# Optimization experiments

Measured on AMD Instinct MI355X. Metric: run time of the kernel, lower is better.

## Reference

```python
import jax, jax.numpy as jnp
import numpy as np

ACT_BITS = 8
W_BITS = 8
BN_EPS = 1e-5


def _round_ste(x):
    # straight-through round (HAWQ-style ste_round)
    return x + jax.lax.stop_gradient(jnp.round(x) - x)


def _quant_sym(x, bits):
    # symmetric per-tensor fake quantization; scale treated as constant (EMA min/max in original)
    n = float(2 ** (bits - 1) - 1)
    s = jax.lax.stop_gradient(jnp.maximum(jnp.max(jnp.abs(x)) / n, 1e-8))
    xq = jnp.clip(_round_ste(x / s), -n - 1.0, n) * s
    return xq, s


def _conv(x, w, stride, pad):
    return jax.lax.conv_general_dilated(
        x, w, (stride, stride), [(pad, pad), (pad, pad)],
        dimension_numbers=("NCHW", "OIHW", "NCHW"))


def _quant_bn(x, gamma, beta, mean, var):
    # fold BN into a per-channel scale+bias; quantize the folded scale like a weight
    ws = gamma * jax.lax.rsqrt(var + BN_EPS)          # [C]
    wq, ws_scale = _quant_sym(ws, W_BITS)
    b = beta - mean * wq                               # [C]
    return x * wq[None, :, None, None] + b[None, :, None, None], ws_scale


def setup_inputs() -> dict:
    key = jax.random.key(0)
    ks = jax.random.split(key, 16)
    d = {}
    d["x"] = jax.random.normal(ks[0], (32, 128, 56, 56), jnp.float32)
    d["w1"] = jax.random.normal(ks[1], (256, 128, 3, 3), jnp.float32) * 0.05
    d["w2"] = jax.random.normal(ks[2], (256, 256, 3, 3), jnp.float32) * 0.05
    d["w_id"] = jax.random.normal(ks[3], (256, 128, 1, 1), jnp.float32) * 0.05
    for i, pfx in enumerate(["bn1", "bn2", "id"]):
        k4 = jax.random.split(ks[4 + i], 4)
        d[pfx + "_gamma"] = jax.random.uniform(k4[0], (256,), jnp.float32) + 0.5
        d[pfx + "_beta"] = jax.random.normal(k4[1], (256,), jnp.float32) * 0.1
        d[pfx + "_mean"] = jax.random.normal(k4[2], (256,), jnp.float32) * 0.1
        d[pfx + "_var"] = jax.random.uniform(k4[3], (256,), jnp.float32) + 0.5
    return d


def reference(x, w1, w2, w_id,
              bn1_gamma, bn1_beta, bn1_mean, bn1_var,
              bn2_gamma, bn2_beta, bn2_mean, bn2_var,
              id_gamma, id_beta, id_mean, id_var):
    # quant_act on block input
    xq, act_s = _quant_sym(x, ACT_BITS)

    # identity branch: 1x1 stride-2 quantized conv -> quant_act -> folded quant bn
    w_id_q, _ = _quant_sym(w_id, W_BITS)
    identity = _conv(xq, w_id_q, 2, 0)
    identity, _ = _quant_sym(identity, ACT_BITS)
    identity, _ = _quant_bn(identity, id_gamma, id_beta, id_mean, id_var)

    # main branch conv1 (3x3 stride 2) -> act quant -> bn -> relu -> act quant
    w1_q, _ = _quant_sym(w1, W_BITS)
    h = _conv(xq, w1_q, 2, 1)
    h, _ = _quant_sym(h, ACT_BITS)
    h, _ = _quant_bn(h, bn1_gamma, bn1_beta, bn1_mean, bn1_var)
    h = jax.nn.relu(h)
    h, _ = _quant_sym(h, ACT_BITS)

    # conv2 (3x3 stride 1) -> act quant -> bn
    w2_q, _ = _quant_sym(w2, W_BITS)
    h = _conv(h, w2_q, 1, 1)
    h, _ = _quant_sym(h, ACT_BITS)
    h, _ = _quant_bn(h, bn2_gamma, bn2_beta, bn2_mean, bn2_var)

    # residual add -> int32 requant -> relu
    h = h + identity
    h, out_s = _quant_sym(h, ACT_BITS)
    h = jax.nn.relu(h)
    return h, out_s
```

## Files before the change

### kernel.cpp

```cpp
#include <hip/hip_runtime.h>
#include <limits.h>

#define THREADS 256
#define GRID_BLOCKS 896

typedef int vi4 __attribute__((ext_vector_type(4)));

__device__ __forceinline__ float clamp8f(float q) { return fminf(fmaxf(q, -128.0f), 127.0f); }
__device__ __forceinline__ float sc_from_bits(unsigned b) {
  return fmaxf(__uint_as_float(b) / 127.0f, 1e-8f);
}
__device__ __forceinline__ signed char q8(float v, float s) {
  return (signed char)(int)clamp8f(rintf(v / s));
}


__device__ __forceinline__ void gbar(int* IS, int base, int bx) {
  asm volatile("s_waitcnt vmcnt(0)" ::: "memory");
  int old = __hip_atomic_fetch_add(IS + base + (bx & 7) * 16, 1, __ATOMIC_RELAXED,
                                   __HIP_MEMORY_SCOPE_AGENT);
  if (old == 111) {
    int r = __hip_atomic_fetch_add(IS + base + 128, 1, __ATOMIC_RELAXED, __HIP_MEMORY_SCOPE_AGENT);
    if (r == 7)
      __hip_atomic_fetch_add(IS + base + 144, 1, __ATOMIC_RELAXED, __HIP_MEMORY_SCOPE_AGENT);
  }
  while (__hip_atomic_load(IS + base + 144, __ATOMIC_RELAXED, __HIP_MEMORY_SCOPE_SYSTEM) == 0)
    __builtin_amdgcn_s_sleep(2);
}

__device__ __forceinline__ void amax_body(const float4* __restrict__ p, int n4, int bid,
                                          int nblocks, int* __restrict__ slot) {
  const int tid = threadIdx.x;
  const int stride = nblocks * THREADS;
  float m = 0.0f;
  int i = bid * THREADS + tid;
  for (; i + 3 * stride < n4; i += 4 * stride) {
    float4 v0 = p[i];
    float4 v1 = p[i + stride];
    float4 v2 = p[i + 2 * stride];
    float4 v3 = p[i + 3 * stride];
    float m0 = fmaxf(fmaxf(fabsf(v0.x), fabsf(v0.y)), fmaxf(fabsf(v0.z), fabsf(v0.w)));
    float m1 = fmaxf(fmaxf(fabsf(v1.x), fabsf(v1.y)), fmaxf(fabsf(v1.z), fabsf(v1.w)));
    float m2 = fmaxf(fmaxf(fabsf(v2.x), fabsf(v2.y)), fmaxf(fabsf(v2.z), fabsf(v2.w)));
    float m3 = fmaxf(fmaxf(fabsf(v3.x), fabsf(v3.y)), fmaxf(fabsf(v3.z), fabsf(v3.w)));
    m = fmaxf(m, fmaxf(fmaxf(m0, m1), fmaxf(m2, m3)));
  }
  for (; i < n4; i += stride) {
    float4 v = p[i];
    m = fmaxf(m, fmaxf(fmaxf(fabsf(v.x), fabsf(v.y)), fmaxf(fabsf(v.z), fabsf(v.w))));
  }
#pragma unroll
  for (int k = 32; k >= 1; k >>= 1) m = fmaxf(m, __shfl_xor(m, k));
  __shared__ float wred[4];
  if ((tid & 63) == 0) wred[tid >> 6] = m;
  __syncthreads();
  if (tid == 0) {
    m = fmaxf(fmaxf(wred[0], wred[1]), fmaxf(wred[2], wred[3]));
    atomicMax(slot, __float_as_int(m));
  }
}

__global__ __launch_bounds__(THREADS) void k_pre(
    int* IS, const float* g1, const float* be1, const float* m1, const float* v1, float* wq1,
    float* b1, const float* g2, const float* be2, const float* m2, const float* v2, float* wq2,
    float* b2, const float* gi, const float* bei, const float* mi, const float* vvi, float* wqi,
    float* bi, const float4* w1, const float4* w2, const float4* wid, const float4* x) {
  int b = blockIdx.x;
  int c = threadIdx.x;
  if (b < 3) {
    if (b == 0) {
      IS[128 + c] = 0;
      IS[384 + c] = 0;
      IS[640 + c] = 0;
      if (c < 32) IS[896 + c] = 0;
    }
    const float *gamma, *beta, *mean, *var;
    float *wq, *bb;
    if (b == 0) { gamma = g1; beta = be1; mean = m1; var = v1; wq = wq1; bb = b1; }
    else if (b == 1) { gamma = g2; beta = be2; mean = m2; var = v2; wq = wq2; bb = b2; }
    else { gamma = gi; beta = bei; mean = mi; var = vvi; wq = wqi; bb = bi; }
    __shared__ float red[THREADS];
    float ws = gamma[c] * (1.0f / sqrtf(var[c] + 1e-5f));
    red[c] = fabsf(ws);
    __syncthreads();
    for (int s = THREADS / 2; s > 0; s >>= 1) {
      if (c < s) red[c] = fmaxf(red[c], red[c + s]);
      __syncthreads();
    }
    float sws = fmaxf(red[0] / 127.0f, 1e-8f);
    float q = clamp8f(rintf(ws / sws)) * sws;
    wq[c] = q;
    bb[c] = beta[c] - mean[c] * q;
    return;
  }
  b -= 3;
  if (b < 64) { amax_body(w1, 73728, b, 64, IS + 1); return; }
  b -= 64;
  if (b < 128) { amax_body(w2, 147456, b, 128, IS + 2); return; }
  b -= 128;
  if (b < 16) { amax_body(wid, 8192, b, 16, IS + 3); return; }
  b -= 16;
  amax_body(x, 3211264, b, 512, IS + 0);
}

__global__ __launch_bounds__(THREADS) void k_quant(const float* __restrict__ x,
                                                   int* __restrict__ X8,
                                                   const float* __restrict__ w1f,
                                                   vi4* __restrict__ W1m,
                                                   const float* __restrict__ w2f,
                                                   vi4* __restrict__ W2m,
                                                   const float* __restrict__ widf,
                                                   vi4* __restrict__ Widm,
                                                   const unsigned* __restrict__ ISu) {
  __shared__ signed char tile[56 * 132];
  int b = blockIdx.x;
  int t = threadIdx.x;
  if (b < 1792) {
    float s = sc_from_bits(ISu[0]);
    int h = b % 56, n = b / 56;
    const float* xp = x + ((n * 128) * 56 + h) * 56;
#pragma unroll
    for (int k = 0; k < 28; ++k) {
      int i = t + k * 256;
      int w = i % 56, c = i / 56;
      tile[w * 132 + c] = q8(xp[c * 3136 + w], s);
    }
    __syncthreads();
    int* op = X8 + (n * 56 + h) * 56 * 32;
#pragma unroll
    for (int k = 0; k < 7; ++k) {
      int i = t + k * 256;
      int w = i >> 5, c4 = (i & 31) * 4;
      const signed char* tp = tile + w * 132 + c4;
      op[i] = (int)(unsigned char)tp[0] | ((int)(unsigned char)tp[1] << 8) |
              ((int)(unsigned char)tp[2] << 16) | ((int)(unsigned char)tp[3] << 24);
    }
    return;
  }
  if (b < 1864) {
    int tt = (b - 1792) * THREADS + t;
    float s = sc_from_bits(ISu[1]);
    int lane = tt & 63;
    int cotile = (tt >> 6) & 15;
    int ks = tt >> 10;
    int tap = ks >> 1, kc = ks & 1;
    int kh = tap / 3, kw = tap % 3;
    int co = cotile * 16 + (lane & 15);
    int ci0 = kc * 64 + (lane >> 4) * 16;
    const float* src = w1f + (co * 128 + ci0) * 9 + kh * 3 + kw;
    int r[4];
#pragma unroll
    for (int q = 0; q < 4; ++q) {
      unsigned b0 = (unsigned char)q8(src[(q * 4 + 0) * 9], s);
      unsigned b1 = (unsigned char)q8(src[(q * 4 + 1) * 9], s);
      unsigned b2 = (unsigned char)q8(src[(q * 4 + 2) * 9], s);
      unsigned b3 = (unsigned char)q8(src[(q * 4 + 3) * 9], s);
      r[q] = (int)(b0 | (b1 << 8) | (b2 << 16) | (b3 << 24));
    }
    vi4 v = {r[0], r[1], r[2], r[3]};
    W1m[tt] = v;
    return;
  }
  if (b < 2008) {
    int tt = (b - 1864) * THREADS + t;
    float s = sc_from_bits(ISu[2]);
    int lane = tt & 63;
    int cotile = (tt >> 6) & 15;
    int ks = tt >> 10;
    int tap = ks >> 2, kc = ks & 3;
    int kh = tap / 3, kw = tap % 3;
    int co = cotile * 16 + (lane & 15);
    int ci0 = kc * 64 + (lane >> 4) * 16;
    const float* src = w2f + (co * 256 + ci0) * 9 + kh * 3 + kw;
    int r[4];
#pragma unroll
    for (int q = 0; q < 4; ++q) {
      unsigned b0 = (unsigned char)q8(src[(q * 4 + 0) * 9], s);
      unsigned b1 = (unsigned char)q8(src[(q * 4 + 1) * 9], s);
      unsigned b2 = (unsigned char)q8(src[(q * 4 + 2) * 9], s);
      unsigned b3 = (unsigned char)q8(src[(q * 4 + 3) * 9], s);
      r[q] = (int)(b0 | (b1 << 8) | (b2 << 16) | (b3 << 24));
    }
    vi4 v = {r[0], r[1], r[2], r[3]};
    W2m[tt] = v;
    return;
  }
  {
    int tt = (b - 2008) * THREADS + t;
    float s = sc_from_bits(ISu[3]);
    int lane = tt & 63;
    int cotile = (tt >> 6) & 15;
    int ks = tt >> 10;
    int co = cotile * 16 + (lane & 15);
    int ci0 = ks * 64 + (lane >> 4) * 16;
    const float* src = widf + co * 128 + ci0;
    int r[4];
#pragma unroll
    for (int q = 0; q < 4; ++q) {
      unsigned b0 = (unsigned char)q8(src[q * 4 + 0], s);
      unsigned b1 = (unsigned char)q8(src[q * 4 + 1], s);
      unsigned b2 = (unsigned char)q8(src[q * 4 + 2], s);
      unsigned b3 = (unsigned char)q8(src[q * 4 + 3], s);
      r[q] = (int)(b0 | (b1 << 8) | (b2 << 16) | (b3 << 24));
    }
    vi4 v = {r[0], r[1], r[2], r[3]};
    Widm[tt] = v;
  }
}

#define MFMA_I8(a, b, c) __builtin_amdgcn_mfma_i32_16x16x64_i8(a, b, c, 0, 0, 0)

__device__ __forceinline__ signed char qact(int v, float sxw, float s_h1, float s_y2, float wq,
                                            float bb) {
  float hf = (float)v * sxw;
  float q = clamp8f(rintf(hf / s_h1));
  float hv = q * s_h1;
  float y = fmaxf(hv * wq + bb, 0.0f);
  float a = fminf(fmaxf(rintf(y / s_y2), -128.0f), 127.0f);
  return (signed char)(int)a;
}

__device__ __forceinline__ float sc_slot(const int* IS, int slot) {
  unsigned u = (unsigned)__hip_atomic_load((int*)(IS + slot), __ATOMIC_RELAXED,
                                           __HIP_MEMORY_SCOPE_AGENT);
  return fmaxf(__uint_as_float(u) / 127.0f, 1e-8f);
}

__global__ __launch_bounds__(THREADS, 4) void k_cv1(const int* X8, const vi4* __restrict__ W1m,
                                                    const vi4* __restrict__ Widm,
                                                    int* __restrict__ IDI, int* A2i, int* IS,
                                                    const float* __restrict__ wq1,
                                                    const float* __restrict__ b1, float* SC,
                                                    int* maxS2, int* minS2) {
  __shared__ __align__(16) int lds[9280];
  __shared__ int redA[4];
  __shared__ int sVmax, sVmin;
  __shared__ float sSxw, sSh1, sSy2;
  const int tid = threadIdx.x;
  const int bx = blockIdx.x;
  const int n = bx / 28, rr = bx % 28;
  const int hp = rr >> 1, nh = rr & 1;
  const int ho0 = hp * 2;
  vi4 zero = {0, 0, 0, 0};

  for (int r = 0; r < 5; ++r) {
    int h = 2 * ho0 - 1 + r;
    int* dst = lds + r * 58 * 32;
    if (h >= 0 && h < 56) {
      const vi4* src = (const vi4*)(X8 + (n * 56 + h) * 56 * 32);
      for (int i4 = tid; i4 < 448; i4 += THREADS) {
        int col = i4 >> 3, e0 = (i4 & 7) * 4;
        int cell = r * 58 + col + 1;
        *(vi4*)(lds + cell * 32 + (e0 ^ ((cell & 7) << 2))) = src[i4];
      }
      if (tid < 32) dst[tid] = 0;
      else if (tid >= 128 && tid < 160) dst[57 * 32 + (tid - 128)] = 0;
    } else {
      for (int i4 = tid; i4 < 464; i4 += THREADS) ((vi4*)dst)[i4] = zero;
    }
  }
  __syncthreads();

  const int lane = tid & 63, wv = tid >> 6;
  const int mw = wv & 1, nw = wv >> 1;
  const int lm = lane & 15, quad = lane >> 4;
  const int woc0 = lm, woc1 = (16 + lm) > 27 ? 27 : (16 + lm);
  const int choff = quad * 4;
  const int ho = ho0 + mw;
  const int obase = ((n * 28 + ho) * 28) * 256;
  const int ctbase = nh * 8 + nw * 4;

#define LDA(row, colp, sub)                                                              \
  (*(const vi4*)(lds + ((row) * 58 + (colp)) * 32 +                                      \
                 ((sub) ^ ((((row) * 58 + (colp)) & 7) << 2))))

  vi4 acc[2][4];
  vi4 bA[4], bB[4];
  vi4 a0A, a1A, a0B, a1B;

#pragma unroll
  for (int mt = 0; mt < 2; ++mt)
#pragma unroll
    for (int ct = 0; ct < 4; ++ct) acc[mt][ct] = zero;
  const vi4* wibase = Widm + ctbase * 64 + lane;
  {
    const int row = 2 * mw + 1;
#pragma unroll
    for (int kc = 0; kc < 2; ++kc) {
      vi4 a0 = LDA(row, 2 * woc0 + 1, kc * 16 + choff);
      vi4 a1 = LDA(row, 2 * woc1 + 1, kc * 16 + choff);
#pragma unroll
      for (int ct = 0; ct < 4; ++ct) {
        vi4 b = wibase[kc * 1024 + ct * 64];
        acc[0][ct] = MFMA_I8(a0, b, acc[0][ct]);
        acc[1][ct] = MFMA_I8(a1, b, acc[1][ct]);
      }
    }
  }
  int am = 0;
#pragma unroll
  for (int ct = 0; ct < 4; ++ct) {
    const int co = (ctbase + ct) * 16 + lm;
#pragma unroll
    for (int mt = 0; mt < 2; ++mt)
#pragma unroll
      for (int r = 0; r < 4; ++r) {
        int wo = mt * 16 + quad * 4 + r;
        if (wo < 28) {
          int v = acc[mt][ct][r];
          IDI[obase + wo * 256 + co] = v;
          am = max(am, v < 0 ? -v : v);
        }
      }
  }
#pragma unroll
  for (int k = 32; k >= 1; k >>= 1) am = max(am, __shfl_xor(am, k));
  if (lane == 0) redA[wv] = am;

#pragma unroll
  for (int mt = 0; mt < 2; ++mt)
#pragma unroll
    for (int ct = 0; ct < 4; ++ct) acc[mt][ct] = zero;
  const vi4* wbase = W1m + ctbase * 64 + lane;
#pragma unroll
  for (int ct = 0; ct < 4; ++ct) bA[ct] = wbase[ct * 64];
  {
    a0A = LDA(2 * mw, 2 * woc0, choff);
    a1A = LDA(2 * mw, 2 * woc1, choff);
  }
#pragma unroll 1
  for (int ks = 0; ks < 18; ks += 2) {
    {
      const int ksn = ks + 1;
      const int khn = (ksn >= 6) + (ksn >= 12);
      const int t2 = ksn - khn * 6;
      const int kwn = t2 >> 1, kcn = t2 & 1;
#pragma unroll
      for (int ct = 0; ct < 4; ++ct) bB[ct] = wbase[ksn * 1024 + ct * 64];
      const int row = 2 * mw + khn;
      a0B = LDA(row, 2 * woc0 + kwn, kcn * 16 + choff);
      a1B = LDA(row, 2 * woc1 + kwn, kcn * 16 + choff);
    }
#pragma unroll
    for (int ct = 0; ct < 4; ++ct) {
      acc[0][ct] = MFMA_I8(a0A, bA[ct], acc[0][ct]);
      acc[1][ct] = MFMA_I8(a1A, bA[ct], acc[1][ct]);
    }
    if (ks + 2 < 18) {
      const int ksn = ks + 2;
      const int khn = (ksn >= 6) + (ksn >= 12);
      const int t2 = ksn - khn * 6;
      const int kwn = t2 >> 1, kcn = t2 & 1;
#pragma unroll
      for (int ct = 0; ct < 4; ++ct) bA[ct] = wbase[ksn * 1024 + ct * 64];
      const int row = 2 * mw + khn;
      a0A = LDA(row, 2 * woc0 + kwn, kcn * 16 + choff);
      a1A = LDA(row, 2 * woc1 + kwn, kcn * 16 + choff);
    }
#pragma unroll
    for (int ct = 0; ct < 4; ++ct) {
      acc[0][ct] = MFMA_I8(a0B, bB[ct], acc[0][ct]);
      acc[1][ct] = MFMA_I8(a1B, bB[ct], acc[1][ct]);
    }
  }

#pragma unroll
  for (int ct = 0; ct < 4; ++ct) {
    int vmax = INT_MIN, vmin = INT_MAX;
#pragma unroll
    for (int mt = 0; mt < 2; ++mt)
#pragma unroll
      for (int r = 0; r < 4; ++r) {
        int wo = mt * 16 + quad * 4 + r;
        if (wo < 28) {
          int v = acc[mt][ct][r];
          vmax = max(vmax, v);
          vmin = min(vmin, v);
        }
      }
    vmax = max(vmax, __shfl_xor(vmax, 16));
    vmax = max(vmax, __shfl_xor(vmax, 32));
    vmin = min(vmin, __shfl_xor(vmin, 16));
    vmin = min(vmin, __shfl_xor(vmin, 32));
    if (lane < 16) {
      int cl = (nw * 4 + ct) * 16 + lane;
      __hip_atomic_store(maxS2 + bx * 256 + mw * 128 + cl, vmax, __ATOMIC_RELAXED,
                         __HIP_MEMORY_SCOPE_AGENT);
      __hip_atomic_store(minS2 + bx * 256 + mw * 128 + cl, vmin, __ATOMIC_RELAXED,
                         __HIP_MEMORY_SCOPE_AGENT);
    }
  }

  __syncthreads();
  if (tid == 0) {
    int a = max(max(redA[0], redA[1]), max(redA[2], redA[3]));
    atomicMax(IS + 5, a);
  }
#pragma unroll
  for (int ct = 0; ct < 4; ++ct) {
    const int cl = (nw * 4 + ct) * 16 + lm;
#pragma unroll
    for (int mt = 0; mt < 2; ++mt)
#pragma unroll
      for (int r = 0; r < 4; ++r) {
        int wo = mt * 16 + quad * 4 + r;
        if (wo < 28) lds[(mw * 28 + wo) * 130 + cl] = acc[mt][ct][r];
      }
  }
  __syncthreads();
  if (tid == 0) gbar(IS, 128, bx);
  __syncthreads();

  if (bx < 256) {
    const int c = bx, nhc = c >> 7, cl = c & 127;
    int vmax = INT_MIN, vmin = INT_MAX;
    for (int j = tid; j < 896; j += THREADS) {
      int bxx = nhc + ((j >> 1) << 1);
      int mwj = j & 1;
      int a = __hip_atomic_load(maxS2 + bxx * 256 + mwj * 128 + cl, __ATOMIC_RELAXED,
                                __HIP_MEMORY_SCOPE_AGENT);
      int i_ = __hip_atomic_load(minS2 + bxx * 256 + mwj * 128 + cl, __ATOMIC_RELAXED,
                                 __HIP_MEMORY_SCOPE_AGENT);
      vmax = max(vmax, a);
      vmin = min(vmin, i_);
    }
    int* rMax = lds + 7280;
    int* rMin = lds + 7536;
    rMax[tid] = vmax;
    rMin[tid] = vmin;
    __syncthreads();
    for (int s = 128; s > 0; s >>= 1) {
      if (tid < s) {
        rMax[tid] = max(rMax[tid], rMax[tid + s]);
        rMin[tid] = min(rMin[tid], rMin[tid + s]);
      }
      __syncthreads();
    }
    if (tid == 0) {
      sVmax = rMax[0];
      sVmin = rMin[0];
      int a1 = sVmax < 0 ? -sVmax : sVmax;
      int a0 = sVmin < 0 ? -sVmin : sVmin;
      atomicMax(IS + 4, max(a1, a0));
    }
  }
  __syncthreads();
  if (tid == 0) gbar(IS, 288, bx);
  __syncthreads();

  if (bx < 256 && tid == 0) {
    float sx = sc_slot(IS, 0);
    float sw1 = sc_slot(IS, 1);
    int mh1 = __hip_atomic_load(IS + 4, __ATOMIC_RELAXED, __HIP_MEMORY_SCOPE_AGENT);
    float sxw = sx * sw1;
    float s_h1 = fmaxf(sxw * (float)mh1 / 127.0f, 1e-8f);
    float wq = wq1[bx], bbc = b1[bx];
    float q1 = clamp8f(rintf((float)sVmax * sxw / s_h1));
    float q0 = clamp8f(rintf((float)sVmin * sxw / s_h1));
    float y1 = fmaxf(q1 * s_h1 * wq + bbc, 0.0f);
    float y0 = fmaxf(q0 * s_h1 * wq + bbc, 0.0f);
    atomicMax(IS + 7, __float_as_int(fmaxf(y1, y0)));
  }
  __syncthreads();
  if (tid == 0) gbar(IS, 448, bx);
  __syncthreads();

  if (tid == 0) {
    float sx = sc_slot(IS, 0);
    float sw1 = sc_slot(IS, 1);
    int mh1 = __hip_atomic_load(IS + 4, __ATOMIC_RELAXED, __HIP_MEMORY_SCOPE_AGENT);
    int mrf = __hip_atomic_load(IS + 7, __ATOMIC_RELAXED, __HIP_MEMORY_SCOPE_AGENT);
    float sxw = sx * sw1;
    float s_h1 = fmaxf(sxw * (float)mh1 / 127.0f, 1e-8f);
    float s_y2 = fmaxf(__int_as_float(mrf) / 127.0f, 1e-8f);
    sSxw = sxw;
    sSh1 = s_h1;
    sSy2 = s_y2;
    if (bx == 0) {
      int mid = __hip_atomic_load(IS + 5, __ATOMIC_RELAXED, __HIP_MEMORY_SCOPE_AGENT);
      float swid = sc_slot(IS, 3);
      SC[9] = s_y2;
      SC[10] = fmaxf(sx * swid * (float)mid / 127.0f, 1e-8f);
    }
  }
  __syncthreads();

  {
    const float sxw = sSxw, s_h1 = sSh1, s_y2 = sSy2;
#pragma unroll
    for (int k = 0; k < 7; ++k) {
      int i = tid + k * 256;
      int sp = i >> 5, c4i = i & 31;
      int mwp = sp >= 28 ? 1 : 0;
      int wo = sp - mwp * 28;
      int c0 = nh * 128 + c4i * 4;
      const int* pk = lds + sp * 130 + c4i * 4;
      unsigned r0 = (unsigned char)qact(pk[0], sxw, s_h1, s_y2, wq1[c0], b1[c0]);
      unsigned r1 = (unsigned char)qact(pk[1], sxw, s_h1, s_y2, wq1[c0 + 1], b1[c0 + 1]);
      unsigned r2 = (unsigned char)qact(pk[2], sxw, s_h1, s_y2, wq1[c0 + 2], b1[c0 + 2]);
      unsigned r3 = (unsigned char)qact(pk[3], sxw, s_h1, s_y2, wq1[c0 + 3], b1[c0 + 3]);
      A2i[((n * 28 + ho0 + mwp) * 28 + wo) * 64 + nh * 32 + c4i] =
          (int)(r0 | (r1 << 8) | (r2 << 16) | (r3 << 24));
    }
  }
#undef LDA
}

struct SumParams {
  float sxw2, s_h2, sxwid, s_idq;
};
__device__ __forceinline__ float sum_val(int v2, int vi, const SumParams& P, float wq2c, float b2c,
                                         float wqidc, float bidc) {
  float q2 = clamp8f(rintf((float)v2 * P.sxw2 / P.s_h2));
  float z = (q2 * P.s_h2) * wq2c + b2c;
  float qi = clamp8f(rintf((float)vi * P.sxwid / P.s_idq));
  float zi = (qi * P.s_idq) * wqidc + bidc;
  return z + zi;
}
__device__ __forceinline__ SumParams make_params2(const float* SC, const unsigned* ISu, int mh2) {
  SumParams P;
  float sx = sc_from_bits(ISu[0]);
  float sw2 = sc_from_bits(ISu[2]);
  float swid = sc_from_bits(ISu[3]);
  float s_y2 = SC[9];
  P.s_idq = SC[10];
  P.sxw2 = s_y2 * sw2;
  P.s_h2 = fmaxf(P.sxw2 * (float)mh2 / 127.0f, 1e-8f);
  P.sxwid = sx * swid;
  return P;
}

__global__ __launch_bounds__(THREADS, 4) void k_tail(const int* __restrict__ A2,
                                                     const vi4* __restrict__ W2m,
                                                     const int* __restrict__ IDI,
                                                     const float* SC, int* IS,
                                                     const float* __restrict__ wq2,
                                                     const float* __restrict__ b2,
                                                     const float* __restrict__ wqid,
                                                     const float* __restrict__ bidp,
                                                     float* __restrict__ out) {
  __shared__ __align__(16) int lds[4 * 30 * 68];
  __shared__ int redA[4];
  __shared__ float redF[4];
  __shared__ int sMh2;
  __shared__ float sOutS;
  const int tid = threadIdx.x;
  const int bx = blockIdx.x;
  const int n = bx / 28, rr = bx % 28;
  const int hp = rr >> 1, nh = rr & 1;
  const int ho0 = hp * 2;
  vi4 zero = {0, 0, 0, 0};

  for (int r = 0; r < 4; ++r) {
    int h = ho0 - 1 + r;
    int* dst = lds + r * 30 * 68;
    if (h >= 0 && h < 28) {
      const vi4* src = (const vi4*)(A2 + (n * 28 + h) * 28 * 64);
      for (int i4 = tid; i4 < 448; i4 += THREADS) {
        int col = i4 >> 4, c = (i4 & 15) * 4;
        *(vi4*)(dst + (col + 1) * 68 + c) = src[i4];
      }
      if (tid < 64) dst[tid] = 0;
      else if (tid >= 128 && tid < 192) dst[29 * 68 + (tid - 128)] = 0;
    } else {
      for (int i4 = tid; i4 < 510; i4 += THREADS) ((vi4*)dst)[i4] = zero;
    }
  }
  __syncthreads();

  const int lane = tid & 63, wv = tid >> 6;
  const int mw = wv & 1, nw = wv >> 1;
  const int lm = lane & 15, quad = lane >> 4;
  const int woc0 = lm, woc1 = (16 + lm) > 27 ? 27 : (16 + lm);
  const int choff = quad * 4;
  const int ctbase = nh * 8 + nw * 4;

  vi4 acc[2][4];
  vi4 bA[4], bB[4];
  vi4 a0A, a1A, a0B, a1B;
#pragma unroll
  for (int mt = 0; mt < 2; ++mt)
#pragma unroll
    for (int ct = 0; ct < 4; ++ct) acc[mt][ct] = zero;

  const vi4* wbase = W2m + ctbase * 64 + lane;
#pragma unroll
  for (int ct = 0; ct < 4; ++ct) bA[ct] = wbase[ct * 64];
  {
    const int ro = mw * 30;
    a0A = *(const vi4*)(lds + (ro + woc0) * 68 + choff);
    a1A = *(const vi4*)(lds + (ro + woc1) * 68 + choff);
  }
#pragma unroll 1
  for (int ks = 0; ks < 36; ks += 2) {
    {
      const int ksn = ks + 1;
      const int khn = (ksn >= 12) + (ksn >= 24);
      const int t2 = ksn - khn * 12;
      const int kwn = t2 >> 2, kcn = t2 & 3;
#pragma unroll
      for (int ct = 0; ct < 4; ++ct) bB[ct] = wbase[ksn * 1024 + ct * 64];
      const int ro = (mw + khn) * 30;
      a0B = *(const vi4*)(lds + (ro + woc0 + kwn) * 68 + kcn * 16 + choff);
      a1B = *(const vi4*)(lds + (ro + woc1 + kwn) * 68 + kcn * 16 + choff);
    }
#pragma unroll
    for (int ct = 0; ct < 4; ++ct) {
      acc[0][ct] = MFMA_I8(a0A, bA[ct], acc[0][ct]);
      acc[1][ct] = MFMA_I8(a1A, bA[ct], acc[1][ct]);
    }
    if (ks + 2 < 36) {
      const int ksn = ks + 2;
      const int khn = (ksn >= 12) + (ksn >= 24);
      const int t2 = ksn - khn * 12;
      const int kwn = t2 >> 2, kcn = t2 & 3;
#pragma unroll
      for (int ct = 0; ct < 4; ++ct) bA[ct] = wbase[ksn * 1024 + ct * 64];
      const int ro = (mw + khn) * 30;
      a0A = *(const vi4*)(lds + (ro + woc0 + kwn) * 68 + kcn * 16 + choff);
      a1A = *(const vi4*)(lds + (ro + woc1 + kwn) * 68 + kcn * 16 + choff);
    }
#pragma unroll
    for (int ct = 0; ct < 4; ++ct) {
      acc[0][ct] = MFMA_I8(a0B, bB[ct], acc[0][ct]);
      acc[1][ct] = MFMA_I8(a1B, bB[ct], acc[1][ct]);
    }
  }

  int am = 0;
#pragma unroll
  for (int ct = 0; ct < 4; ++ct)
#pragma unroll
    for (int mt = 0; mt < 2; ++mt)
#pragma unroll
      for (int r = 0; r < 4; ++r) {
        int wo = mt * 16 + quad * 4 + r;
        if (wo < 28) {
          int v = acc[mt][ct][r];
          am = max(am, v < 0 ? -v : v);
        }
      }
#pragma unroll
  for (int k = 32; k >= 1; k >>= 1) am = max(am, __shfl_xor(am, k));
  if (lane == 0) redA[wv] = am;
  __syncthreads();
  if (tid == 0) {
    int a = max(max(redA[0], redA[1]), max(redA[2], redA[3]));
    atomicMax(IS + 6, a);
  }

  int* sumsi = lds;
  float* sums = (float*)lds;
  const int ib = ((n * 28 + ho0) * 28) * 256 + nh * 128;
#pragma unroll
  for (int k = 0; k < 28; ++k) {
    int idx = tid + k * 256;
    int cl = idx & 127, sp = idx >> 7;
    sumsi[cl * 57 + sp] = IDI[ib + sp * 256 + cl];
  }
  __syncthreads();
  if (tid == 0) {
    gbar(IS, 608, bx);
    sMh2 = __hip_atomic_load(IS + 6, __ATOMIC_RELAXED, __HIP_MEMORY_SCOPE_SYSTEM);
  }
  __syncthreads();
  const SumParams P = make_params2(SC, (const unsigned*)IS, sMh2);

  float fm = 0.0f;
#pragma unroll
  for (int ct = 0; ct < 4; ++ct) {
    const int co = (ctbase + ct) * 16 + lm;
    const int cl = co - nh * 128;
    float w2c = wq2[co], b2c = b2[co], wic = wqid[co], bic = bidp[co];
#pragma unroll
    for (int mt = 0; mt < 2; ++mt)
#pragma unroll
      for (int r = 0; r < 4; ++r) {
        int wo = mt * 16 + quad * 4 + r;
        if (wo < 28) {
          int slot = cl * 57 + mw * 28 + wo;
          float sv = sum_val(acc[mt][ct][r], sumsi[slot], P, w2c, b2c, wic, bic);
          sums[slot] = sv;
          fm = fmaxf(fm, fabsf(sv));
        }
      }
  }
#pragma unroll
  for (int k = 32; k >= 1; k >>= 1) fm = fmaxf(fm, __shfl_xor(fm, k));
  if (lane == 0) redF[wv] = fm;
  __syncthreads();
  if (tid == 0) {
    float a = fmaxf(fmaxf(redF[0], redF[1]), fmaxf(redF[2], redF[3]));
    atomicMax(IS + 11, __float_as_int(a));
    gbar(IS, 768, bx);
    int mb = __hip_atomic_load(IS + 11, __ATOMIC_RELAXED, __HIP_MEMORY_SCOPE_SYSTEM);
    sOutS = fmaxf(__int_as_float(mb) / 127.0f, 1e-8f);
  }
  __syncthreads();
  const float out_s = sOutS;

  float* ob = out + n * 200704 + (nh * 128) * 784 + ho0 * 28;
#pragma unroll
  for (int k = 0; k < 28; ++k) {
    int idx = tid + k * 256;
    int cl = idx / 56, rem = idx % 56;
    float sv = sums[cl * 57 + rem];
    float q = clamp8f(rintf(sv / out_s));
    ob[cl * 784 + rem] = q > 0.0f ? q * out_s : 0.0f;
  }
  if (bx == 0 && tid == 0) out[6422528] = out_s;
}

extern "C" void kernel_launch(void* const* d_in, const int* in_sizes, int n_in, void* d_out,
                              int out_size, void* d_ws, size_t ws_size, hipStream_t stream) {
  (void)in_sizes; (void)n_in; (void)out_size; (void)ws_size;
  const float* x = (const float*)d_in[0];
  const float* w1 = (const float*)d_in[1];
  const float* w2 = (const float*)d_in[2];
  const float* wid = (const float*)d_in[3];
  const float* bn1g = (const float*)d_in[4];
  const float* bn1b = (const float*)d_in[5];
  const float* bn1m = (const float*)d_in[6];
  const float* bn1v = (const float*)d_in[7];
  const float* bn2g = (const float*)d_in[8];
  const float* bn2b = (const float*)d_in[9];
  const float* bn2m = (const float*)d_in[10];
  const float* bn2v = (const float*)d_in[11];
  const float* idg = (const float*)d_in[12];
  const float* idb = (const float*)d_in[13];
  const float* idm = (const float*)d_in[14];
  const float* idv = (const float*)d_in[15];

  char* ws = (char*)d_ws;
  float* SC = (float*)ws;
  int* IS = (int*)ws;
  unsigned* ISu = (unsigned*)ws;
  float* wq1 = (float*)(ws + 4096);
  float* b1 = (float*)(ws + 5120);
  float* wq2 = (float*)(ws + 6144);
  float* b2 = (float*)(ws + 7168);
  float* wqid = (float*)(ws + 8192);
  float* bid = (float*)(ws + 9216);
  char* X8 = ws + 16384;
  char* A2 = X8;
  char* W1m = X8 + 12845056;
  char* W2m = W1m + 294912;
  char* Widm = W2m + 589824;
  int* IDI = (int*)(Widm + 32768);
  float* out = (float*)d_out;
  int* maxS2 = (int*)d_out;
  int* minS2 = maxS2 + 896 * 256;

  k_pre<<<723, THREADS, 0, stream>>>(IS, bn1g, bn1b, bn1m, bn1v, wq1, b1, bn2g, bn2b, bn2m, bn2v,
                                     wq2, b2, idg, idb, idm, idv, wqid, bid, (const float4*)w1,
                                     (const float4*)w2, (const float4*)wid, (const float4*)x);
  k_quant<<<2016, THREADS, 0, stream>>>(x, (int*)X8, w1, (vi4*)W1m, w2, (vi4*)W2m, wid,
                                        (vi4*)Widm, ISu);
  k_cv1<<<GRID_BLOCKS, THREADS, 0, stream>>>((const int*)X8, (const vi4*)W1m, (const vi4*)Widm,
                                             IDI, (int*)A2, IS, wq1, b1, SC, maxS2, minS2);
  k_tail<<<GRID_BLOCKS, THREADS, 0, stream>>>((const int*)A2, (const vi4*)W2m, (const int*)IDI, SC,
                                              IS, wq2, b2, wqid, bid, out);
}
```

Measured before the change: 249.8 us.

## Fuse conv1 and tail kernels into one persistent kernel, keep identity in registers

Merges the conv1 kernel and the conv2/residual tail kernel into a single persistent kernel. A grid barrier separates the A2 activation write from the conv2 halo read. The identity-branch int32 accumulators now stay in registers across the whole kernel instead of round-tripping through the IDI global buffer, and the scale parameters stay in shared memory instead of the SC slots. This removes one kernel launch and the IDI write and read traffic, in exchange for higher register pressure from the extra accumulators and an added grid-wide barrier that relies on all 896 blocks being co-resident.

```diff
diff --git a/kernel.cpp b/kernel.cpp
--- a/kernel.cpp
+++ b/kernel.cpp
@@ -72,7 +72,7 @@
       IS[128 + c] = 0;
       IS[384 + c] = 0;
       IS[640 + c] = 0;
-      if (c < 32) IS[896 + c] = 0;
+      if (c < 192) IS[896 + c] = 0;
     }
     const float *gamma, *beta, *mean, *var;
     float *wq, *bb;
@@ -226,16 +226,31 @@
   return fmaxf(__uint_as_float(u) / 127.0f, 1e-8f);
 }
 
-__global__ __launch_bounds__(THREADS, 4) void k_cv1(const int* X8, const vi4* __restrict__ W1m,
-                                                    const vi4* __restrict__ Widm,
-                                                    int* __restrict__ IDI, int* A2i, int* IS,
-                                                    const float* __restrict__ wq1,
-                                                    const float* __restrict__ b1, float* SC,
-                                                    int* maxS2, int* minS2) {
+struct SumParams {
+  float sxw2, s_h2, sxwid, s_idq;
+};
+__device__ __forceinline__ float sum_val(int v2, int vi, const SumParams& P, float wq2c, float b2c,
+                                         float wqidc, float bidc) {
+  float q2 = clamp8f(rintf((float)v2 * P.sxw2 / P.s_h2));
+  float z = (q2 * P.s_h2) * wq2c + b2c;
+  float qi = clamp8f(rintf((float)vi * P.sxwid / P.s_idq));
+  float zi = (qi * P.s_idq) * wqidc + bidc;
+  return z + zi;
+}
+
+__global__ __launch_bounds__(THREADS, 4) void k_ct(
+    const int* X8, const vi4* __restrict__ W1m, const vi4* __restrict__ Widm,
+    const vi4* __restrict__ W2m, int* A2p, int* IS, const float* __restrict__ wq1,
+    const float* __restrict__ b1, const float* __restrict__ wq2, const float* __restrict__ b2,
+    const float* __restrict__ wqid, const float* __restrict__ bidp, float* __restrict__ out,
+    int* maxS2, int* minS2) {
   __shared__ __align__(16) int lds[9280];
-  __shared__ int redA[4];
+  __shared__ int redA[4], redH[4];
   __shared__ int sVmax, sVmin;
-  __shared__ float sSxw, sSh1, sSy2;
+  __shared__ float redF[4];
+  __shared__ float sSxw, sSh1, sSy2, sSxwid, sSidq, sSxw2;
+  __shared__ int sMh2;
+  __shared__ float sOutS;
   const int tid = threadIdx.x;
   const int bx = blockIdx.x;
   const int n = bx / 28, rr = bx % 28;
@@ -266,8 +281,6 @@
   const int lm = lane & 15, quad = lane >> 4;
   const int woc0 = lm, woc1 = (16 + lm) > 27 ? 27 : (16 + lm);
   const int choff = quad * 4;
-  const int ho = ho0 + mw;
-  const int obase = ((n * 28 + ho) * 28) * 256;
   const int ctbase = nh * 8 + nw * 4;
 
 #define LDA(row, colp, sub)                                                              \
@@ -275,13 +288,14 @@
                  ((sub) ^ ((((row) * 58 + (colp)) & 7) << 2))))
 
   vi4 acc[2][4];
+  vi4 accI[2][4];
   vi4 bA[4], bB[4];
   vi4 a0A, a1A, a0B, a1B;
 
 #pragma unroll
   for (int mt = 0; mt < 2; ++mt)
 #pragma unroll
-    for (int ct = 0; ct < 4; ++ct) acc[mt][ct] = zero;
+    for (int ct = 0; ct < 4; ++ct) accI[mt][ct] = zero;
   const vi4* wibase = Widm + ctbase * 64 + lane;
   {
     const int row = 2 * mw + 1;
@@ -292,27 +306,24 @@
 #pragma unroll
       for (int ct = 0; ct < 4; ++ct) {
         vi4 b = wibase[kc * 1024 + ct * 64];
-        acc[0][ct] = MFMA_I8(a0, b, acc[0][ct]);
-        acc[1][ct] = MFMA_I8(a1, b, acc[1][ct]);
+        accI[0][ct] = MFMA_I8(a0, b, accI[0][ct]);
+        accI[1][ct] = MFMA_I8(a1, b, accI[1][ct]);
       }
     }
   }
   int am = 0;
 #pragma unroll
-  for (int ct = 0; ct < 4; ++ct) {
-    const int co = (ctbase + ct) * 16 + lm;
+  for (int ct = 0; ct < 4; ++ct)
 #pragma unroll
     for (int mt = 0; mt < 2; ++mt)
 #pragma unroll
       for (int r = 0; r < 4; ++r) {
         int wo = mt * 16 + quad * 4 + r;
         if (wo < 28) {
-          int v = acc[mt][ct][r];
-          IDI[obase + wo * 256 + co] = v;
+          int v = accI[mt][ct][r];
           am = max(am, v < 0 ? -v : v);
         }
       }
-  }
 #pragma unroll
   for (int k = 32; k >= 1; k >>= 1) am = max(am, __shfl_xor(am, k));
   if (lane == 0) redA[wv] = am;
@@ -363,6 +374,7 @@
       acc[1][ct] = MFMA_I8(a1B, bB[ct], acc[1][ct]);
     }
   }
+#undef LDA
 
 #pragma unroll
   for (int ct = 0; ct < 4; ++ct) {
@@ -471,17 +483,15 @@
     int mh1 = __hip_atomic_load(IS + 4, __ATOMIC_RELAXED, __HIP_MEMORY_SCOPE_AGENT);
     int mrf = __hip_atomic_load(IS + 7, __ATOMIC_RELAXED, __HIP_MEMORY_SCOPE_AGENT);
     float sxw = sx * sw1;
-    float s_h1 = fmaxf(sxw * (float)mh1 / 127.0f, 1e-8f);
+    sSxw = sxw;
+    sSh1 = fmaxf(sxw * (float)mh1 / 127.0f, 1e-8f);
     float s_y2 = fmaxf(__int_as_float(mrf) / 127.0f, 1e-8f);
-    sSxw = sxw;
-    sSh1 = s_h1;
     sSy2 = s_y2;
-    if (bx == 0) {
-      int mid = __hip_atomic_load(IS + 5, __ATOMIC_RELAXED, __HIP_MEMORY_SCOPE_AGENT);
-      float swid = sc_slot(IS, 3);
-      SC[9] = s_y2;
-      SC[10] = fmaxf(sx * swid * (float)mid / 127.0f, 1e-8f);
-    }
+    int mid = __hip_atomic_load(IS + 5, __ATOMIC_RELAXED, __HIP_MEMORY_SCOPE_AGENT);
+    float swid = sc_slot(IS, 3);
+    sSxwid = sx * swid;
+    sSidq = fmaxf(sx * swid * (float)mid / 127.0f, 1e-8f);
+    sSxw2 = s_y2 * sc_slot(IS, 2);
   }
   __syncthreads();
 
@@ -499,63 +509,20 @@
       unsigned r1 = (unsigned char)qact(pk[1], sxw, s_h1, s_y2, wq1[c0 + 1], b1[c0 + 1]);
       unsigned r2 = (unsigned char)qact(pk[2], sxw, s_h1, s_y2, wq1[c0 + 2], b1[c0 + 2]);
       unsigned r3 = (unsigned char)qact(pk[3], sxw, s_h1, s_y2, wq1[c0 + 3], b1[c0 + 3]);
-      A2i[((n * 28 + ho0 + mwp) * 28 + wo) * 64 + nh * 32 + c4i] =
-          (int)(r0 | (r1 << 8) | (r2 << 16) | (r3 << 24));
-    }
-  }
-#undef LDA
-}
-
-struct SumParams {
-  float sxw2, s_h2, sxwid, s_idq;
-};
-__device__ __forceinline__ float sum_val(int v2, int vi, const SumParams& P, float wq2c, float b2c,
-                                         float wqidc, float bidc) {
-  float q2 = clamp8f(rintf((float)v2 * P.sxw2 / P.s_h2));
-  float z = (q2 * P.s_h2) * wq2c + b2c;
-  float qi = clamp8f(rintf((float)vi * P.sxwid / P.s_idq));
-  float zi = (qi * P.s_idq) * wqidc + bidc;
-  return z + zi;
-}
-__device__ __forceinline__ SumParams make_params2(const float* SC, const unsigned* ISu, int mh2) {
-  SumParams P;
-  float sx = sc_from_bits(ISu[0]);
-  float sw2 = sc_from_bits(ISu[2]);
-  float swid = sc_from_bits(ISu[3]);
-  float s_y2 = SC[9];
-  P.s_idq = SC[10];
-  P.sxw2 = s_y2 * sw2;
-  P.s_h2 = fmaxf(P.sxw2 * (float)mh2 / 127.0f, 1e-8f);
-  P.sxwid = sx * swid;
-  return P;
-}
-
-__global__ __launch_bounds__(THREADS, 4) void k_tail(const int* __restrict__ A2,
-                                                     const vi4* __restrict__ W2m,
-                                                     const int* __restrict__ IDI,
-                                                     const float* SC, int* IS,
-                                                     const float* __restrict__ wq2,
-                                                     const float* __restrict__ b2,
-                                                     const float* __restrict__ wqid,
-                                                     const float* __restrict__ bidp,
-                                                     float* __restrict__ out) {
-  __shared__ __align__(16) int lds[4 * 30 * 68];
-  __shared__ int redA[4];
-  __shared__ float redF[4];
-  __shared__ int sMh2;
-  __shared__ float sOutS;
-  const int tid = threadIdx.x;
-  const int bx = blockIdx.x;
-  const int n = bx / 28, rr = bx % 28;
-  const int hp = rr >> 1, nh = rr & 1;
-  const int ho0 = hp * 2;
-  vi4 zero = {0, 0, 0, 0};
+      __hip_atomic_store(A2p + ((n * 28 + ho0 + mwp) * 28 + wo) * 64 + nh * 32 + c4i,
+                         (int)(r0 | (r1 << 8) | (r2 << 16) | (r3 << 24)), __ATOMIC_RELAXED,
+                         __HIP_MEMORY_SCOPE_AGENT);
+    }
+  }
+  __syncthreads();
+  if (tid == 0) gbar(IS, 608, bx);
+  __syncthreads();
 
   for (int r = 0; r < 4; ++r) {
     int h = ho0 - 1 + r;
     int* dst = lds + r * 30 * 68;
     if (h >= 0 && h < 28) {
-      const vi4* src = (const vi4*)(A2 + (n * 28 + h) * 28 * 64);
+      const vi4* src = (const vi4*)(A2p + (n * 28 + h) * 28 * 64);
       for (int i4 = tid; i4 < 448; i4 += THREADS) {
         int col = i4 >> 4, c = (i4 & 15) * 4;
         *(vi4*)(dst + (col + 1) * 68 + c) = src[i4];
@@ -568,24 +535,13 @@
   }
   __syncthreads();
 
-  const int lane = tid & 63, wv = tid >> 6;
-  const int mw = wv & 1, nw = wv >> 1;
-  const int lm = lane & 15, quad = lane >> 4;
-  const int woc0 = lm, woc1 = (16 + lm) > 27 ? 27 : (16 + lm);
-  const int choff = quad * 4;
-  const int ctbase = nh * 8 + nw * 4;
-
-  vi4 acc[2][4];
-  vi4 bA[4], bB[4];
-  vi4 a0A, a1A, a0B, a1B;
 #pragma unroll
   for (int mt = 0; mt < 2; ++mt)
 #pragma unroll
     for (int ct = 0; ct < 4; ++ct) acc[mt][ct] = zero;
-
-  const vi4* wbase = W2m + ctbase * 64 + lane;
-#pragma unroll
-  for (int ct = 0; ct < 4; ++ct) bA[ct] = wbase[ct * 64];
+  const vi4* wbase2 = W2m + ctbase * 64 + lane;
+#pragma unroll
+  for (int ct = 0; ct < 4; ++ct) bA[ct] = wbase2[ct * 64];
   {
     const int ro = mw * 30;
     a0A = *(const vi4*)(lds + (ro + woc0) * 68 + choff);
@@ -599,7 +555,7 @@
       const int t2 = ksn - khn * 12;
       const int kwn = t2 >> 2, kcn = t2 & 3;
 #pragma unroll
-      for (int ct = 0; ct < 4; ++ct) bB[ct] = wbase[ksn * 1024 + ct * 64];
+      for (int ct = 0; ct < 4; ++ct) bB[ct] = wbase2[ksn * 1024 + ct * 64];
       const int ro = (mw + khn) * 30;
       a0B = *(const vi4*)(lds + (ro + woc0 + kwn) * 68 + kcn * 16 + choff);
       a1B = *(const vi4*)(lds + (ro + woc1 + kwn) * 68 + kcn * 16 + choff);
@@ -615,7 +571,7 @@
       const int t2 = ksn - khn * 12;
       const int kwn = t2 >> 2, kcn = t2 & 3;
 #pragma unroll
-      for (int ct = 0; ct < 4; ++ct) bA[ct] = wbase[ksn * 1024 + ct * 64];
+      for (int ct = 0; ct < 4; ++ct) bA[ct] = wbase2[ksn * 1024 + ct * 64];
       const int ro = (mw + khn) * 30;
       a0A = *(const vi4*)(lds + (ro + woc0 + kwn) * 68 + kcn * 16 + choff);
       a1A = *(const vi4*)(lds + (ro + woc1 + kwn) * 68 + kcn * 16 + choff);
@@ -627,7 +583,7 @@
     }
   }
 
-  int am = 0;
+  int am2 = 0;
 #pragma unroll
   for (int ct = 0; ct < 4; ++ct)
 #pragma unroll
@@ -637,35 +593,27 @@
         int wo = mt * 16 + quad * 4 + r;
         if (wo < 28) {
           int v = acc[mt][ct][r];
-          am = max(am, v < 0 ? -v : v);
+          am2 = max(am2, v < 0 ? -v : v);
         }
       }
 #pragma unroll
-  for (int k = 32; k >= 1; k >>= 1) am = max(am, __shfl_xor(am, k));
-  if (lane == 0) redA[wv] = am;
+  for (int k = 32; k >= 1; k >>= 1) am2 = max(am2, __shfl_xor(am2, k));
+  if (lane == 0) redH[wv] = am2;
   __syncthreads();
   if (tid == 0) {
-    int a = max(max(redA[0], redA[1]), max(redA[2], redA[3]));
-    atomicMax(IS + 6, a);
-  }
-
-  int* sumsi = lds;
+    atomicMax(IS + 6, max(max(redH[0], redH[1]), max(redH[2], redH[3])));
+    gbar(IS, 768, bx);
+    sMh2 = __hip_atomic_load(IS + 6, __ATOMIC_RELAXED, __HIP_MEMORY_SCOPE_SYSTEM);
+  }
+  __syncthreads();
+
+  SumParams P;
+  P.sxw2 = sSxw2;
+  P.s_h2 = fmaxf(sSxw2 * (float)sMh2 / 127.0f, 1e-8f);
+  P.sxwid = sSxwid;
+  P.s_idq = sSidq;
+
   float* sums = (float*)lds;
-  const int ib = ((n * 28 + ho0) * 28) * 256 + nh * 128;
-#pragma unroll
-  for (int k = 0; k < 28; ++k) {
-    int idx = tid + k * 256;
-    int cl = idx & 127, sp = idx >> 7;
-    sumsi[cl * 57 + sp] = IDI[ib + sp * 256 + cl];
-  }
-  __syncthreads();
-  if (tid == 0) {
-    gbar(IS, 608, bx);
-    sMh2 = __hip_atomic_load(IS + 6, __ATOMIC_RELAXED, __HIP_MEMORY_SCOPE_SYSTEM);
-  }
-  __syncthreads();
-  const SumParams P = make_params2(SC, (const unsigned*)IS, sMh2);
-
   float fm = 0.0f;
 #pragma unroll
   for (int ct = 0; ct < 4; ++ct) {
@@ -679,7 +627,7 @@
         int wo = mt * 16 + quad * 4 + r;
         if (wo < 28) {
           int slot = cl * 57 + mw * 28 + wo;
-          float sv = sum_val(acc[mt][ct][r], sumsi[slot], P, w2c, b2c, wic, bic);
+          float sv = sum_val(acc[mt][ct][r], accI[mt][ct][r], P, w2c, b2c, wic, bic);
           sums[slot] = sv;
           fm = fmaxf(fm, fabsf(sv));
         }
@@ -692,7 +640,7 @@
   if (tid == 0) {
     float a = fmaxf(fmaxf(redF[0], redF[1]), fmaxf(redF[2], redF[3]));
     atomicMax(IS + 11, __float_as_int(a));
-    gbar(IS, 768, bx);
+    gbar(IS, 928, bx);
     int mb = __hip_atomic_load(IS + 11, __ATOMIC_RELAXED, __HIP_MEMORY_SCOPE_SYSTEM);
     sOutS = fmaxf(__int_as_float(mb) / 127.0f, 1e-8f);
   }
@@ -732,21 +680,19 @@
   const float* idv = (const float*)d_in[15];
 
   char* ws = (char*)d_ws;
-  float* SC = (float*)ws;
   int* IS = (int*)ws;
   unsigned* ISu = (unsigned*)ws;
-  float* wq1 = (float*)(ws + 4096);
-  float* b1 = (float*)(ws + 5120);
-  float* wq2 = (float*)(ws + 6144);
-  float* b2 = (float*)(ws + 7168);
-  float* wqid = (float*)(ws + 8192);
-  float* bid = (float*)(ws + 9216);
+  float* wq1 = (float*)(ws + 4608);
+  float* b1 = (float*)(ws + 5632);
+  float* wq2 = (float*)(ws + 6656);
+  float* b2 = (float*)(ws + 7680);
+  float* wqid = (float*)(ws + 8704);
+  float* bid = (float*)(ws + 9728);
   char* X8 = ws + 16384;
-  char* A2 = X8;
   char* W1m = X8 + 12845056;
   char* W2m = W1m + 294912;
   char* Widm = W2m + 589824;
-  int* IDI = (int*)(Widm + 32768);
+  int* A2p = (int*)(Widm + 32768);
   float* out = (float*)d_out;
   int* maxS2 = (int*)d_out;
   int* minS2 = maxS2 + 896 * 256;
@@ -756,8 +702,7 @@
                                      (const float4*)w2, (const float4*)wid, (const float4*)x);
   k_quant<<<2016, THREADS, 0, stream>>>(x, (int*)X8, w1, (vi4*)W1m, w2, (vi4*)W2m, wid,
                                         (vi4*)Widm, ISu);
-  k_cv1<<<GRID_BLOCKS, THREADS, 0, stream>>>((const int*)X8, (const vi4*)W1m, (const vi4*)Widm,
-                                             IDI, (int*)A2, IS, wq1, b1, SC, maxS2, minS2);
-  k_tail<<<GRID_BLOCKS, THREADS, 0, stream>>>((const int*)A2, (const vi4*)W2m, (const int*)IDI, SC,
-                                              IS, wq2, b2, wqid, bid, out);
-}
+  k_ct<<<GRID_BLOCKS, THREADS, 0, stream>>>((const int*)X8, (const vi4*)W1m, (const vi4*)Widm,
+                                            (const vi4*)W2m, A2p, IS, wq1, b1, wq2, b2, wqid, bid,
+                                            out, maxS2, minS2);
+}
```

New measurement: 238.7 us, median of 2. 1.05x faster.
